# Kernel optimization log

Measured on AMD Instinct MI355X. Metric: run time of the kernel, lower is better.

The kernel has to match this reference:

```python
import jax, jax.numpy as jnp
import numpy as np

PI = 3.141592653589793


def conv2d(x, w, b=None, padding=0, groups=1):
    out = jax.lax.conv_general_dilated(
        x, w, window_strides=(1, 1), padding=((padding, padding), (padding, padding)),
        dimension_numbers=('NCHW', 'OIHW', 'NCHW'), feature_group_count=groups)
    if b is not None:
        out = out + b.reshape(1, -1, 1, 1)
    return out


def group_norm(x, weight, bias, num_groups, eps=1e-5):
    B, C, H, W = x.shape
    xg = x.reshape(B, num_groups, C // num_groups, H, W)
    mean = xg.mean(axis=(2, 3, 4), keepdims=True)
    var = xg.var(axis=(2, 3, 4), keepdims=True)
    xg = (xg - mean) / jnp.sqrt(var + eps)
    return xg.reshape(B, C, H, W) * weight.reshape(1, -1, 1, 1) + bias.reshape(1, -1, 1, 1)


def l2norm(x, eps=1e-12):
    n = jnp.sqrt(jnp.sum(x * x, axis=1, keepdims=True))
    return x / jnp.maximum(n, eps)


def dense_sift(x):
    # kornia DenseSIFTDescriptor defaults: 8 angle bins, 4x4 spatial bins, bin size 4,
    # stride 1, padding 1, rootsift=True, clipval=0.2. Input (B,1,H,W) -> (B,128,H,W).
    eps = 1e-10
    B, C, H, W = x.shape
    # spatial_gradient(x, 'diff'), normalized: central differences / 2, replicate pad
    p = jnp.pad(x, ((0, 0), (0, 0), (1, 1), (1, 1)), mode='edge')
    gx = (p[:, :, 1:-1, 2:] - p[:, :, 1:-1, :-2]) * 0.5
    gy = (p[:, :, 2:, 1:-1] - p[:, :, :-2, 1:-1]) * 0.5
    mag = jnp.sqrt(gx * gx + gy * gy + eps)
    ori = jnp.arctan2(gy, gx + eps) + 2.0 * PI
    o_big = 8.0 * ori / (2.0 * PI)
    bo0f = jnp.floor(o_big)
    wo1 = o_big - bo0f
    bo0 = bo0f % 8
    bo1 = (bo0 + 1) % 8
    wo0m = (1.0 - wo1) * mag
    wo1m = wo1 * mag
    bins = jnp.arange(8, dtype=x.dtype).reshape(1, 8, 1, 1)
    # soft orientation-histogram binning -> (B,8,H,W)
    ang = jnp.where(bo0 == bins, wo0m, 0.0) + jnp.where(bo1 == bins, wo1m, 0.0)
    # triangular bin pooling kernel (ksize=4), depthwise conv, pad 2 -> (B,8,H+1,W+1)
    ks2 = 2.0
    xc2 = ks2 - jnp.abs(jnp.arange(4, dtype=x.dtype) + 0.5 - ks2)
    pk = jnp.outer(xc2, xc2) / (ks2 ** 2)
    pk = jnp.tile(pk.reshape(1, 1, 4, 4), (8, 1, 1, 1))
    pooled = jax.lax.conv_general_dilated(
        ang, pk, (1, 1), ((2, 2), (2, 2)),
        dimension_numbers=('NCHW', 'OIHW', 'NCHW'), feature_group_count=8)
    # PoolingConv with identity reshape kernel (k=4, pad=1) == 4x4 patch extraction
    pp = jnp.pad(pooled, ((0, 0), (0, 0), (1, 1), (1, 1)))
    patches = jnp.stack([pp[:, :, y:y + H, xx:xx + W]
                         for y in range(4) for xx in range(4)], axis=2)  # (B,8,16,H,W)
    out = patches.reshape(B, 128, H, W)
    out = jnp.clip(l2norm(out), 0.0, 0.2)
    out = l2norm(out)
    # rootsift: sqrt(L1-normalized + eps)
    l1 = jnp.sum(jnp.abs(out), axis=1, keepdims=True)
    out = jnp.sqrt(out / jnp.maximum(l1, 1e-12) + eps)
    return out


def gauss1d(ks, sigma):
    t = jnp.arange(ks, dtype=jnp.float32) - (ks - 1) / 2.0
    g = jnp.exp(-(t * t) / (2.0 * sigma * sigma))
    return g / g.sum()


def joint_bilateral_blur(inp, guidance, ks=5, sigma_color=0.1, sigma_space=(1.5, 1.5)):
    # kornia joint_bilateral_blur: border_type='reflect', color_distance_type='l1'
    B, C, H, W = inp.shape
    pad = ks // 2
    pi_ = jnp.pad(inp, ((0, 0), (0, 0), (pad, pad), (pad, pad)), mode='reflect')
    pg = jnp.pad(guidance, ((0, 0), (0, 0), (pad, pad), (pad, pad)), mode='reflect')

    def unfold(p):  # (B,C,H,W,ks*ks), flatten order (dy, dx)
        return jnp.stack([p[:, :, y:y + H, x:x + W]
                          for y in range(ks) for x in range(ks)], axis=-1)

    ui = unfold(pi_)
    ug = unfold(pg)
    diff = ug - guidance[..., None]
    cdist_sq = jnp.square(jnp.sum(jnp.abs(diff), axis=1, keepdims=True))  # L1 over channels, squared
    color_k = jnp.exp(-0.5 / (sigma_color ** 2) * cdist_sq)               # (B,1,H,W,K2)
    space_k = jnp.outer(gauss1d(ks, sigma_space[0]), gauss1d(ks, sigma_space[1])).reshape(1, 1, 1, 1, -1)
    kernel = space_k * color_k
    return (ui * kernel).sum(-1) / kernel.sum(-1)


def setup_inputs() -> dict:
    key = jax.random.key(0)
    ks = jax.random.split(key, 8)
    B, H, W = 4, 270, 512

    def wgt(k, shape, scale=0.05):
        return jax.random.normal(k, shape, dtype=jnp.float32) * scale

    z = lambda n: jnp.zeros((n,), dtype=jnp.float32)
    o = lambda n: jnp.ones((n,), dtype=jnp.float32)
    return {
        'x': jax.random.normal(ks[0], (B, 1, H, W), dtype=jnp.float32),
        'w1': wgt(ks[1], (64, 128, 5, 5)), 'b1': z(64), 'g1w': o(64), 'g1b': z(64),
        'w2': wgt(ks[2], (32, 64, 3, 3)), 'b2': z(32), 'g2w': o(32), 'g2b': z(32),
        'w3': wgt(ks[3], (16, 32, 3, 3)), 'b3': z(16), 'g3w': o(16), 'g3b': z(16),
        'w4': wgt(ks[4], (8, 16, 3, 3)), 'b4': z(8), 'g4w': o(8), 'g4b': z(8),
        'w5': wgt(ks[5], (2, 8, 3, 3)), 'b5': z(2),
        'sw1': wgt(ks[6], (32, 128, 1, 1)), 'sb1': z(32),
        'sw2': wgt(ks[7], (8, 32, 1, 1)), 'sb2': z(8),
    }


def reference(x, w1, b1, g1w, g1b, w2, b2, g2w, g2b, w3, b3, g3w, g3b,
              w4, b4, g4w, g4b, w5, b5, sw1, sb1, sw2, sb2):
    orig = x
    s = dense_sift(x)                                     # (B,128,H,W)
    h = jax.nn.relu(group_norm(conv2d(s, w1, b1, 2), g1w, g1b, 8))
    h = jax.nn.relu(group_norm(conv2d(h, w2, b2, 1), g2w, g2b, 8))
    h = h + conv2d(s, sw1, sb1, 0)                        # skip 1
    blk = h
    h = jax.nn.relu(group_norm(conv2d(h, w3, b3, 1), g3w, g3b, 4))
    h = jax.nn.relu(group_norm(conv2d(h, w4, b4, 1), g4w, g4b, 4))
    h = h + conv2d(blk, sw2, sb2, 0)                      # skip 2
    h = conv2d(h, w5, b5, 1)                              # (B,2,H,W)
    guide = jnp.tile(orig, (1, 2, 1, 1))
    h = joint_bilateral_blur(h, guide, ks=5, sigma_color=0.1, sigma_space=(1.5, 1.5))
    h = jnp.tanh(h)
    scale = jnp.array([0.436, 0.615], dtype=h.dtype).reshape(1, 2, 1, 1)
    return h * scale
```

## Files before the change

### kernel.cpp

```cpp
#include <hip/hip_runtime.h>

#define DEV __device__ __forceinline__

typedef __bf16 bf16x8 __attribute__((ext_vector_type(8)));
typedef float f32x4 __attribute__((ext_vector_type(4)));

union U8 { uint4 q; unsigned short u[8]; };

constexpr int BN = 4, H = 270, W = 512, HW = H * W;
constexpr int IH5 = 274, P5 = 516;
constexpr int IH3 = 272, P3 = 514;

DEV unsigned short f2bf(float f) {
  unsigned int u = __builtin_bit_cast(unsigned int, f);
  u = (u + 0x7FFFu + ((u >> 16) & 1u)) >> 16;
  return (unsigned short)u;
}
DEV float bf2f(unsigned short h) {
  return __builtin_bit_cast(float, (unsigned int)h << 16);
}

#define GLL16(g, l)                                                                        \
  __builtin_amdgcn_global_load_lds((const __attribute__((address_space(1))) void*)(g),     \
                                   (__attribute__((address_space(3))) void*)(l), 16, 0, 0)

DEV int swz(int row) { return ((row >> 1) & 3) << 4; }

__global__ void k_fill(float* __restrict__ out, int n, float v) {
  int i = blockIdx.x * 256 + threadIdx.x;
  if (i < n) out[i] = v;
}

template <int C, int PD>
__global__ void k_halo(unsigned short* __restrict__ buf, int IHt, int pitch, int nb_) {
  int vPerRow = pitch * C / 8;
  int topBot = 2 * PD * vPerRow;
  int sideV = PD * C / 8;
  int midRows = IHt - 2 * PD;
  int perS = topBot + midRows * 2 * sideV;
  int v = blockIdx.x * 256 + threadIdx.x;
  if (v >= nb_ * perS) return;
  int s = v / perS, r = v % perS;
  size_t base = (size_t)s * IHt * pitch * C;
  size_t off;
  if (r < topBot) {
    int half = r / (PD * vPerRow);
    int rr = r % (PD * vPerRow);
    off = ((size_t)(half ? (IHt - PD) : 0) * pitch * C) + (size_t)rr * 8;
  } else {
    int r2 = r - topBot;
    int row = r2 / (2 * sideV), c2 = r2 % (2 * sideV);
    int side = c2 / sideV, cc = c2 % sideV;
    off = ((size_t)(PD + row) * pitch + (side ? (pitch - PD) : 0)) * C + (size_t)cc * 8;
  }
  *(uint4*)(buf + base + off) = uint4{0, 0, 0, 0};
}

__global__ void k_sift_ang(const float* __restrict__ x, float* __restrict__ ang, int nTot) {
  int p = blockIdx.x * 256 + threadIdx.x;
  if (p >= nTot) return;
  int b = p / HW, r = p % HW, y = r / W, xx = r % W;
  const float* xb = x + (size_t)b * HW;
  float xm = xb[y * W + (xx > 0 ? xx - 1 : 0)];
  float xp = xb[y * W + (xx < W - 1 ? xx + 1 : W - 1)];
  float ym = xb[(y > 0 ? y - 1 : 0) * W + xx];
  float yp = xb[(y < H - 1 ? y + 1 : H - 1) * W + xx];
  float gx = (xp - xm) * 0.5f, gy = (yp - ym) * 0.5f;
  float mag = sqrtf(gx * gx + gy * gy + 1e-10f);
  float ori = atan2f(gy, gx + 1e-10f) + 6.2831855f;
  float o = (8.0f * ori) / 6.2831855f;
  float bo0f = floorf(o);
  float wo1 = o - bo0f;
  int b0 = ((int)bo0f) & 7;
  int b1 = (b0 + 1) & 7;
  float w0m = (1.0f - wo1) * mag, w1m = wo1 * mag;
  float v[8];
#pragma unroll
  for (int k = 0; k < 8; ++k)
    v[k] = (k == b0 ? w0m : 0.0f) + (k == b1 ? w1m : 0.0f);
  float4* o4 = (float4*)(ang + (size_t)p * 8);
  o4[0] = make_float4(v[0], v[1], v[2], v[3]);
  o4[1] = make_float4(v[4], v[5], v[6], v[7]);
}

__global__ void k_sift_pool(const float* __restrict__ ang, float* __restrict__ pooled, int nTot) {
  constexpr int PH = H + 1, PW = W + 1;
  int p = blockIdx.x * 256 + threadIdx.x;
  if (p >= nTot) return;
  int b = p / (PH * PW), r = p % (PH * PW), y = r / PW, xx = r % PW;
  float4 a0 = {0, 0, 0, 0}, a1 = {0, 0, 0, 0};
  const float xc2[4] = {0.5f, 1.5f, 1.5f, 0.5f};
#pragma unroll
  for (int ky = 0; ky < 4; ++ky) {
    int yy = y - 2 + ky;
    if (yy < 0 || yy >= H) continue;
#pragma unroll
    for (int kx = 0; kx < 4; ++kx) {
      int xs = xx - 2 + kx;
      if (xs < 0 || xs >= W) continue;
      float w = xc2[ky] * xc2[kx] * 0.25f;
      const float4* s4 = (const float4*)(ang + ((size_t)(b * H + yy) * W + xs) * 8);
      float4 v0 = s4[0], v1 = s4[1];
      a0.x += w * v0.x; a0.y += w * v0.y; a0.z += w * v0.z; a0.w += w * v0.w;
      a1.x += w * v1.x; a1.y += w * v1.y; a1.z += w * v1.z; a1.w += w * v1.w;
    }
  }
  float4* o4 = (float4*)(pooled + (size_t)p * 8);
  o4[0] = a0; o4[1] = a1;
}

__global__ void k_sift_desc(const float* __restrict__ pooled, unsigned short* __restrict__ spad) {
  constexpr int PH = H + 1, PW = W + 1;
  int tid = threadIdx.x;
  int wv = tid >> 6, lane = tid & 63;
  int p = blockIdx.x * 4 + wv;
  int b = p / HW, r = p % HW, yy = r / W, xx = r % W;
  int a = lane >> 3, jj = lane & 7;
  int j0 = jj * 2;
  int dy = j0 >> 2, dx = j0 & 3;
  int rr = yy + dy - 1;
  int c0 = xx + dx - 1, c1 = c0 + 1;
  bool rv = (rr >= 0 && rr <= H);
  int rc = min(max(rr, 0), H);
  const float* pb = pooled + ((size_t)(b * PH + rc) * PW) * 8 + a;
  float v0 = 0.0f, v1 = 0.0f;
  if (rv && c0 >= 0 && c0 <= W) v0 = pb[(size_t)c0 * 8];
  if (rv && c1 >= 0 && c1 <= W) v1 = pb[(size_t)c1 * 8];

  float n2 = v0 * v0 + v1 * v1;
#pragma unroll
  for (int m = 1; m < 64; m <<= 1) n2 += __shfl_xor(n2, m);
  float inv = 1.0f / fmaxf(sqrtf(n2), 1e-12f);
  v0 = fminf(v0 * inv, 0.2f);
  v1 = fminf(v1 * inv, 0.2f);
  float n2b = v0 * v0 + v1 * v1;
#pragma unroll
  for (int m = 1; m < 64; m <<= 1) n2b += __shfl_xor(n2b, m);
  inv = 1.0f / fmaxf(sqrtf(n2b), 1e-12f);
  v0 *= inv; v1 *= inv;
  float l1 = v0 + v1;
#pragma unroll
  for (int m = 1; m < 64; m <<= 1) l1 += __shfl_xor(l1, m);
  float il1 = 1.0f / fmaxf(l1, 1e-12f);
  v0 = sqrtf(v0 * il1 + 1e-10f);
  v1 = sqrtf(v1 * il1 + 1e-10f);
  unsigned int pk = (unsigned int)f2bf(v0) | ((unsigned int)f2bf(v1) << 16);
  *(unsigned int*)(spad + ((size_t)(b * IH5 + yy + 2) * P5 + xx + 2) * 128 + lane * 2) = pk;
}

template <int CIN, int COUT, int KS>
__global__ void k_prep(const float* __restrict__ w, unsigned short* __restrict__ wbuf) {
  int i = blockIdx.x * 256 + threadIdx.x;
  if (i >= KS * KS * COUT * CIN) return;
  int t = i / (COUT * CIN), r2 = i % (COUT * CIN), co = r2 / CIN, e = r2 % CIN;
  wbuf[i] = f2bf(w[(co * CIN + e) * (KS * KS) + t]);
}

template <int CIN, int COUT, int KS, int NG, int PADOFF, int MINB>
__launch_bounds__(256, MINB)
__global__ void k_convr(const unsigned short* __restrict__ in, int IHt, int ipitch,
                        const unsigned short* __restrict__ wtap,
                        const float* __restrict__ bias,
                        unsigned short* __restrict__ outraw,
                        float* __restrict__ part, int nbid) {
  constexpr int SLABPX = 512 + KS - 1;
  constexpr int KQ = CIN / 32;
  constexpr int NF = COUT / 16;
  constexpr int SLAB = SLABPX * 64;
  constexpr int SWQ = COUT * 64;
  constexpr int SWROW = KS * SWQ;
  __shared__ __align__(16) unsigned char slabB[2][SLAB];
  __shared__ __align__(16) unsigned char wrowB[2][SWROW];
  __shared__ float red[4][16];

  int tid = threadIdx.x;
  int lane = tid & 63, wid = tid >> 6;
  int l15 = lane & 15, hi = lane >> 4;

  int bid = blockIdx.x;
  int q8 = nbid >> 3, r8 = nbid & 7;
  int xcd = bid & 7;
  int by = (xcd < r8 ? xcd * (q8 + 1) : r8 * (q8 + 1) + (xcd - r8) * q8) + (bid >> 3);
  int y = by % H, b = by / H;

  f32x4 acc[8][NF] = {};

  auto stage = [&](int it, int pbuf) {
    int q = it / KS, ky = it % KS;
    const char* src = (const char*)(in + ((size_t)(b * IHt + y + ky + PADOFF) * ipitch + PADOFF) * CIN + q * 32);
    for (int d = tid * 16; d < SLAB; d += 4096) {
      int px = d >> 6, qb = d & 63;
      GLL16(src + px * (CIN * 2) + (qb ^ swz(px)), slabB[pbuf] + d);
    }
    const char* wsrc = (const char*)wtap + (size_t)(ky * KS) * (COUT * CIN * 2) + q * 64;
    for (int d = tid * 16; d < SWROW; d += 4096) {
      int kx = d / SWQ, rem = d % SWQ;
      int co = rem >> 6, qb = rem & 63;
      GLL16(wsrc + (size_t)kx * (COUT * CIN * 2) + co * (CIN * 2) + (qb ^ swz(co)), wrowB[pbuf] + d);
    }
  };

  stage(0, 0);
  __syncthreads();

#pragma unroll 1
  for (int it = 0; it < KQ * KS; ++it) {
    int cur = it & 1;
    if (it + 1 < KQ * KS) stage(it + 1, cur ^ 1);
    const unsigned char* sl = slabB[cur];
    const unsigned char* wr = wrowB[cur];
    int koff = hi * 16;
#pragma unroll
    for (int kx = 0; kx < KS; ++kx) {
      bf16x8 af[8];
#pragma unroll
      for (int mi = 0; mi < 8; ++mi) {
        int px = wid * 128 + mi * 16 + l15 + kx;
        af[mi] = *(const bf16x8*)(sl + px * 64 + (koff ^ swz(px)));
      }
#pragma unroll
      for (int ni = 0; ni < NF; ++ni) {
        int co = ni * 16 + l15;
        bf16x8 bq = *(const bf16x8*)(wr + kx * SWQ + co * 64 + (koff ^ swz(co)));
#pragma unroll
        for (int mi = 0; mi < 8; ++mi)
          acc[mi][ni] = __builtin_amdgcn_mfma_f32_16x16x32_bf16(af[mi], bq, acc[mi][ni], 0, 0, 0);
      }
    }
    __syncthreads();
  }

#pragma unroll
  for (int ni = 0; ni < NF; ++ni) {
    float bv = bias[ni * 16 + l15];
#pragma unroll
    for (int mi = 0; mi < 8; ++mi)
#pragma unroll
      for (int rr = 0; rr < 4; ++rr)
        acc[mi][ni][rr] += bv;
  }
  unsigned short* op = outraw + ((size_t)(b * H + y) * W) * COUT;
#pragma unroll
  for (int mi = 0; mi < 8; ++mi)
#pragma unroll
    for (int rr = 0; rr < 4; ++rr) {
      int px = wid * 128 + mi * 16 + hi * 4 + rr;
#pragma unroll
      for (int ni = 0; ni < NF; ++ni)
        op[(size_t)px * COUT + ni * 16 + l15] = f2bf(acc[mi][ni][rr]);
    }
  if constexpr (NG > 0) {
    constexpr int GPC = COUT / NG;
#pragma unroll
    for (int ni = 0; ni < NF; ++ni) {
      float s = 0.0f, q2 = 0.0f;
#pragma unroll
      for (int mi = 0; mi < 8; ++mi)
#pragma unroll
        for (int rr = 0; rr < 4; ++rr) {
          float v = acc[mi][ni][rr];
          s += v; q2 += v * v;
        }
      s += __shfl_xor(s, 16); q2 += __shfl_xor(q2, 16);
      s += __shfl_xor(s, 32); q2 += __shfl_xor(q2, 32);
#pragma unroll
      for (int m = 1; m < GPC; m <<= 1) { s += __shfl_xor(s, m); q2 += __shfl_xor(q2, m); }
      if (hi == 0 && (l15 % GPC) == 0) {
        int g = ni * (16 / GPC) + l15 / GPC;
        red[wid][g] = s;
        red[wid][NG + g] = q2;
      }
    }
    __syncthreads();
    if (tid < 2 * NG)
      part[(size_t)by * (2 * NG) + tid] =
          red[0][tid] + red[1][tid] + red[2][tid] + red[3][tid];
  }
}

template <int COUT, int NG>
__global__ void k_gn_fin(const float* __restrict__ part, int NB,
                         const float* __restrict__ gw, const float* __restrict__ gb,
                         float* __restrict__ scale, float* __restrict__ shift, float invN) {
  constexpr int GPC = COUT / NG;
  int b = blockIdx.x / NG, g = blockIdx.x % NG;
  int lane = threadIdx.x;
  float s = 0.0f, q = 0.0f;
  for (int i = lane; i < NB; i += 64) {
    const float* pp = part + (size_t)(b * NB + i) * (2 * NG);
    s += pp[g]; q += pp[NG + g];
  }
#pragma unroll
  for (int m = 1; m < 64; m <<= 1) { s += __shfl_xor(s, m); q += __shfl_xor(q, m); }
  if (lane == 0) {
    float mean = s * invN;
    float var = q * invN - mean * mean;
    float rstd = rsqrtf(var + 1e-5f);
#pragma unroll
    for (int j = 0; j < GPC; ++j) {
      int c = g * GPC + j;
      float sc = gw[c] * rstd;
      scale[b * COUT + c] = sc;
      shift[b * COUT + c] = gb[c] - mean * sc;
    }
  }
}

template <int C, bool ADDSKIP>
__global__ void k_norm(const unsigned short* __restrict__ raw,
                       const unsigned short* __restrict__ skip,
                       const float* __restrict__ scale, const float* __restrict__ shift,
                       unsigned short* __restrict__ outpad) {
  int e = blockIdx.x * 256 + threadIdx.x;
  int idx = e * 8;
  int p = idx / C, c0 = idx % C;
  int b = p / HW, r = p % HW, y = r / W, xx = r % W;
  U8 v; v.q = *(const uint4*)(raw + (size_t)p * C + c0);
  U8 sk;
  if (ADDSKIP) sk.q = *(const uint4*)(skip + (size_t)p * C + c0);
  const float* sc = scale + b * C + c0;
  const float* sh = shift + b * C + c0;
  U8 o;
#pragma unroll
  for (int j = 0; j < 8; ++j) {
    float f = fmaxf(bf2f(v.u[j]) * sc[j] + sh[j], 0.0f);
    if (ADDSKIP) f += bf2f(sk.u[j]);
    o.u[j] = f2bf(f);
  }
  *(uint4*)(outpad + ((size_t)(b * IH3 + y + 1) * P3 + xx + 1) * C + c0) = o.q;
}

__global__ void k_conv4(const unsigned short* __restrict__ h3pad, const float* __restrict__ w4,
                        const float* __restrict__ b4, unsigned short* __restrict__ h4raw,
                        float* __restrict__ part) {
  __shared__ float wl[1152];
  __shared__ float red[4][8];
  for (int i = threadIdx.x; i < 1152; i += 256) {
    int t = i / 128, r2 = i % 128, ci = r2 >> 3, co = r2 & 7;
    wl[i] = w4[(co * 16 + ci) * 9 + t];
  }
  __syncthreads();
  int p = blockIdx.x * 256 + threadIdx.x;
  int b = p / HW, r = p % HW, y = r / W, xx = r % W;
  float acc[8];
#pragma unroll
  for (int co = 0; co < 8; ++co) acc[co] = b4[co];
#pragma unroll
  for (int t = 0; t < 9; ++t) {
    int ky = t / 3, kx = t % 3;
    const unsigned short* ip = h3pad + ((size_t)(b * IH3 + y + ky) * P3 + (xx + kx)) * 16;
    U8 u0, u1;
    u0.q = *(const uint4*)ip;
    u1.q = *(const uint4*)(ip + 8);
#pragma unroll
    for (int ci = 0; ci < 16; ++ci) {
      float iv = bf2f(ci < 8 ? u0.u[ci] : u1.u[ci - 8]);
#pragma unroll
      for (int co = 0; co < 8; ++co)
        acc[co] += iv * wl[t * 128 + ci * 8 + co];
    }
  }
  int lane = threadIdx.x & 63, wv = threadIdx.x >> 6;
  float s[4], q[4];
#pragma unroll
  for (int g = 0; g < 4; ++g) {
    s[g] = acc[2 * g] + acc[2 * g + 1];
    q[g] = acc[2 * g] * acc[2 * g] + acc[2 * g + 1] * acc[2 * g + 1];
  }
#pragma unroll
  for (int m = 1; m < 64; m <<= 1) {
#pragma unroll
    for (int g = 0; g < 4; ++g) { s[g] += __shfl_xor(s[g], m); q[g] += __shfl_xor(q[g], m); }
  }
  if (lane == 0) {
#pragma unroll
    for (int g = 0; g < 4; ++g) { red[wv][g] = s[g]; red[wv][4 + g] = q[g]; }
  }
  __syncthreads();
  if (threadIdx.x < 8)
    part[(size_t)blockIdx.x * 8 + threadIdx.x] =
        red[0][threadIdx.x] + red[1][threadIdx.x] + red[2][threadIdx.x] + red[3][threadIdx.x];
  U8 o;
#pragma unroll
  for (int co = 0; co < 8; ++co) o.u[co] = f2bf(acc[co]);
  *(uint4*)(h4raw + (size_t)p * 8) = o.q;
}

__global__ void k_norm4(const unsigned short* __restrict__ h4raw, const unsigned short* __restrict__ blkpad,
                        const float* __restrict__ scale, const float* __restrict__ shift,
                        const float* __restrict__ sw2, const float* __restrict__ sb2,
                        unsigned short* __restrict__ blk2pad) {
  __shared__ float wl[256];
  {
    int i = threadIdx.x;
    int ci = i >> 3, co = i & 7;
    wl[i] = sw2[co * 32 + ci];
  }
  __syncthreads();
  int p = blockIdx.x * 256 + threadIdx.x;
  int b = p / HW, r = p % HW, y = r / W, xx = r % W;
  float acc[8];
#pragma unroll
  for (int co = 0; co < 8; ++co) acc[co] = sb2[co];
  size_t cbase = ((size_t)(b * IH3 + y + 1) * P3 + (xx + 1));
  const unsigned short* bp = blkpad + cbase * 32;
#pragma unroll
  for (int half = 0; half < 4; ++half) {
    U8 u; u.q = *(const uint4*)(bp + half * 8);
#pragma unroll
    for (int j = 0; j < 8; ++j) {
      float iv = bf2f(u.u[j]);
      int ci = half * 8 + j;
#pragma unroll
      for (int co = 0; co < 8; ++co) acc[co] += iv * wl[ci * 8 + co];
    }
  }
  U8 hv; hv.q = *(const uint4*)(h4raw + (size_t)p * 8);
  U8 o;
#pragma unroll
  for (int co = 0; co < 8; ++co) {
    float f = fmaxf(bf2f(hv.u[co]) * scale[b * 8 + co] + shift[b * 8 + co], 0.0f) + acc[co];
    o.u[co] = f2bf(f);
  }
  *(uint4*)(blk2pad + cbase * 8) = o.q;
}

__global__ void k_conv5(const unsigned short* __restrict__ blk2pad, const float* __restrict__ w5,
                        const float* __restrict__ b5, float* __restrict__ h5) {
  __shared__ float wl[144];
  if (threadIdx.x < 144) {
    int i = threadIdx.x;
    int t = i / 16, r2 = i % 16, ci = r2 >> 1, co = r2 & 1;
    wl[i] = w5[(co * 8 + ci) * 9 + t];
  }
  __syncthreads();
  int p = blockIdx.x * 256 + threadIdx.x;
  int b = p / HW, r = p % HW, y = r / W, xx = r % W;
  float a0 = b5[0], a1 = b5[1];
#pragma unroll
  for (int t = 0; t < 9; ++t) {
    int ky = t / 3, kx = t % 3;
    const unsigned short* ip = blk2pad + ((size_t)(b * IH3 + y + ky) * P3 + (xx + kx)) * 8;
    U8 u; u.q = *(const uint4*)ip;
#pragma unroll
    for (int ci = 0; ci < 8; ++ci) {
      float iv = bf2f(u.u[ci]);
      a0 += iv * wl[t * 16 + ci * 2];
      a1 += iv * wl[t * 16 + ci * 2 + 1];
    }
  }
  h5[(size_t)p * 2] = a0;
  h5[(size_t)p * 2 + 1] = a1;
}

__global__ void k_bilateral(const float* __restrict__ h5, const float* __restrict__ x,
                            float* __restrict__ out, int nTot) {
  int p = blockIdx.x * 256 + threadIdx.x;
  if (p >= nTot) return;
  int b = p / HW, r = p % HW, y = r / W, xx = r % W;
  const float* xb = x + (size_t)b * HW;
  float xc = xb[r];
  float e1 = expf(-1.0f / 4.5f), e0 = expf(-4.0f / 4.5f);
  float gs = 1.0f + 2.0f * e1 + 2.0f * e0;
  float g[5] = {e0 / gs, e1 / gs, 1.0f / gs, e1 / gs, e0 / gs};
  float n0 = 0.0f, n1 = 0.0f, den = 0.0f;
#pragma unroll
  for (int dy = 0; dy < 5; ++dy) {
    int yn = y + dy - 2;
    yn = yn < 0 ? -yn : (yn >= H ? 2 * H - 2 - yn : yn);
#pragma unroll
    for (int dx = 0; dx < 5; ++dx) {
      int xn = xx + dx - 2;
      xn = xn < 0 ? -xn : (xn >= W ? 2 * W - 2 - xn : xn);
      float xv = xb[yn * W + xn];
      float d = xv - xc;
      float wgt = g[dy] * g[dx] * expf(-200.0f * d * d);
      den += wgt;
      const float* hp = h5 + ((size_t)(b * HW) + yn * W + xn) * 2;
      n0 += wgt * hp[0];
      n1 += wgt * hp[1];
    }
  }
  float o0 = tanhf(n0 / den) * 0.436f;
  float o1 = tanhf(n1 / den) * 0.615f;
  out[(size_t)(b * 2) * HW + r] = o0;
  out[(size_t)(b * 2 + 1) * HW + r] = o1;
}

extern "C" void kernel_launch(void* const* d_in, const int* in_sizes, int n_in,
                              void* d_out, int out_size, void* d_ws, size_t ws_size,
                              hipStream_t stream) {
  (void)in_sizes; (void)n_in; (void)out_size;
  const float* x   = (const float*)d_in[0];
  const float* w1  = (const float*)d_in[1];
  const float* b1  = (const float*)d_in[2];
  const float* g1w = (const float*)d_in[3];
  const float* g1b = (const float*)d_in[4];
  const float* w2  = (const float*)d_in[5];
  const float* b2  = (const float*)d_in[6];
  const float* g2w = (const float*)d_in[7];
  const float* g2b = (const float*)d_in[8];
  const float* w3  = (const float*)d_in[9];
  const float* b3  = (const float*)d_in[10];
  const float* g3w = (const float*)d_in[11];
  const float* g3b = (const float*)d_in[12];
  const float* w4  = (const float*)d_in[13];
  const float* b4  = (const float*)d_in[14];
  const float* g4w = (const float*)d_in[15];
  const float* g4b = (const float*)d_in[16];
  const float* w5  = (const float*)d_in[17];
  const float* b5  = (const float*)d_in[18];
  const float* sw1 = (const float*)d_in[19];
  const float* sb1 = (const float*)d_in[20];
  const float* sw2 = (const float*)d_in[21];
  const float* sb2 = (const float*)d_in[22];
  float* out = (float*)d_out;
  char* ws = (char*)d_ws;

  auto AL = [](size_t v) { return (v + 255) & ~(size_t)255; };
  const size_t sSPAD  = (size_t)IH5 * P5 * 128 * 2;
  const size_t sANG   = (size_t)HW * 8 * 4;
  const size_t sH1RAW = (size_t)HW * 64 * 2;
  const size_t sH1PAD = (size_t)IH3 * P3 * 64 * 2;
  const size_t sH2RAW = (size_t)HW * 32 * 2;
  const size_t sBLKP  = (size_t)IH3 * P3 * 32 * 2;
  const size_t sH3RAW = (size_t)HW * 16 * 2;
  const size_t sH3PAD = (size_t)IH3 * P3 * 16 * 2;
  const size_t sH4RAW = (size_t)HW * 8 * 2;
  const size_t sBLK2  = (size_t)IH3 * P3 * 8 * 2;

  int nb = 0;
  size_t offB = 0, offH1PAD = 0, offSmall = 0;
  const size_t smallFixed = AL(1024 * 1024) + AL((size_t)4 * 1080 * 16 * 4) + 8 * 4096;
  for (int cand = 4; cand >= 1; cand >>= 1) {
    size_t oB   = AL((size_t)cand * sSPAD);
    size_t oH1P = AL(oB + (size_t)cand * sH1RAW);
    size_t oS   = AL(oH1P + (size_t)cand * sH1PAD);
    size_t need = oS + smallFixed + AL((size_t)cand * sH2RAW);
    if (ws_size >= need) { nb = cand; offB = oB; offH1PAD = oH1P; offSmall = oS; break; }
  }
  if (nb == 0) {
    k_fill<<<(BN * 2 * HW + 255) / 256, 256, 0, stream>>>(out, BN * 2 * HW, 123.0f);
    return;
  }

  size_t oWB1  = offSmall;
  size_t oWB2  = AL(oWB1 + 25 * 64 * 128 * 2);
  size_t oWB3  = AL(oWB2 + 9 * 32 * 64 * 2);
  size_t oWBS  = AL(oWB3 + 9 * 16 * 32 * 2);
  size_t oPART = AL(oWBS + 32 * 128 * 2);
  size_t oSC1  = AL(oPART + (size_t)4 * 1080 * 16 * 4);
  size_t oSC2  = oSC1 + 4096, oSC3 = oSC2 + 4096, oSC4 = oSC3 + 4096;
  size_t oSK1  = oSC4 + 4096;

  unsigned short* wb1  = (unsigned short*)(ws + oWB1);
  unsigned short* wb2  = (unsigned short*)(ws + oWB2);
  unsigned short* wb3  = (unsigned short*)(ws + oWB3);
  unsigned short* wbs1 = (unsigned short*)(ws + oWBS);
  float* part = (float*)(ws + oPART);
  float* sc1 = (float*)(ws + oSC1); float* sh1 = sc1 + nb * 64;
  float* sc2 = (float*)(ws + oSC2); float* sh2 = sc2 + nb * 32;
  float* sc3 = (float*)(ws + oSC3); float* sh3 = sc3 + nb * 16;
  float* sc4 = (float*)(ws + oSC4); float* sh4 = sc4 + nb * 8;
  unsigned short* sk1 = (unsigned short*)(ws + oSK1);

  k_prep<128, 64, 5><<<800, 256, 0, stream>>>(w1, wb1);
  k_prep<64, 32, 3><<<72, 256, 0, stream>>>(w2, wb2);
  k_prep<32, 16, 3><<<18, 256, 0, stream>>>(w3, wb3);
  k_prep<128, 32, 1><<<16, 256, 0, stream>>>(sw1, wbs1);

  size_t t0 = AL((size_t)nb * sBLKP);
  size_t t1 = AL(t0 + (size_t)nb * sH3RAW);
  size_t t2 = AL(t1 + (size_t)nb * sH3PAD);
  size_t t3 = AL(t2 + (size_t)nb * sH4RAW);
  size_t t4 = AL(t3 + (size_t)nb * sBLK2);

  for (int b0 = 0; b0 < BN; b0 += nb) {
    const float* x_c = x + (size_t)b0 * HW;
    float* out_c = out + (size_t)b0 * 2 * HW;
    unsigned short* spad   = (unsigned short*)(ws);
    float*          ang    = (float*)(ws + offB);
    float*          pooled = (float*)(ws + AL(offB + (size_t)nb * sANG));
    unsigned short* h1raw  = (unsigned short*)(ws + offB);
    unsigned short* h1pad  = (unsigned short*)(ws + offH1PAD);
    unsigned short* h2raw  = (unsigned short*)(ws + offB);
    unsigned short* blkpad = (unsigned short*)(ws);
    unsigned short* h3raw  = (unsigned short*)(ws + t0);
    unsigned short* h3pad  = (unsigned short*)(ws + t1);
    unsigned short* h4raw  = (unsigned short*)(ws + t2);
    unsigned short* blk2   = (unsigned short*)(ws + t3);
    float*          h5     = (float*)(ws + t4);
    int nHW = nb * HW;
    int nbid = nb * H;

    k_halo<128, 2><<<(nb * 50304 + 255) / 256, 256, 0, stream>>>(spad, IH5, P5, nb);
    k_halo<64, 1><<<(nb * 12544 + 255) / 256, 256, 0, stream>>>(h1pad, IH3, P3, nb);

    k_sift_ang<<<nb * 540, 256, 0, stream>>>(x_c, ang, nHW);
    int nPP = nb * (H + 1) * (W + 1);
    k_sift_pool<<<(nPP + 255) / 256, 256, 0, stream>>>(ang, pooled, nPP);
    k_sift_desc<<<nHW / 4, 256, 0, stream>>>(pooled, spad);

    k_convr<128, 64, 5, 8, 0, 1><<<nbid, 256, 0, stream>>>(spad, IH5, P5, wb1, b1, h1raw, part, nbid);
    k_gn_fin<64, 8><<<nb * 8, 64, 0, stream>>>(part, H, g1w, g1b, sc1, sh1, 1.0f / (8.0f * HW));
    k_norm<64, false><<<nb * 4320, 256, 0, stream>>>(h1raw, nullptr, sc1, sh1, h1pad);

    k_convr<64, 32, 3, 8, 0, 2><<<nbid, 256, 0, stream>>>(h1pad, IH3, P3, wb2, b2, h2raw, part, nbid);
    k_gn_fin<32, 8><<<nb * 8, 64, 0, stream>>>(part, H, g2w, g2b, sc2, sh2, 1.0f / (4.0f * HW));
    k_convr<128, 32, 1, 0, 2, 2><<<nbid, 256, 0, stream>>>(spad, IH5, P5, wbs1, sb1, sk1, nullptr, nbid);

    k_halo<32, 1><<<(nb * 6272 + 255) / 256, 256, 0, stream>>>(blkpad, IH3, P3, nb);
    k_halo<16, 1><<<(nb * 3136 + 255) / 256, 256, 0, stream>>>(h3pad, IH3, P3, nb);
    k_halo<8, 1><<<(nb * 1568 + 255) / 256, 256, 0, stream>>>(blk2, IH3, P3, nb);

    k_norm<32, true><<<nb * 2160, 256, 0, stream>>>(h2raw, sk1, sc2, sh2, blkpad);

    k_convr<32, 16, 3, 4, 0, 2><<<nbid, 256, 0, stream>>>(blkpad, IH3, P3, wb3, b3, h3raw, part, nbid);
    k_gn_fin<16, 4><<<nb * 4, 64, 0, stream>>>(part, H, g3w, g3b, sc3, sh3, 1.0f / (4.0f * HW));
    k_norm<16, false><<<nb * 1080, 256, 0, stream>>>(h3raw, nullptr, sc3, sh3, h3pad);

    k_conv4<<<nb * 540, 256, 0, stream>>>(h3pad, w4, b4, h4raw, part);
    k_gn_fin<8, 4><<<nb * 4, 64, 0, stream>>>(part, 540, g4w, g4b, sc4, sh4, 1.0f / (2.0f * HW));
    k_norm4<<<nb * 540, 256, 0, stream>>>(h4raw, blkpad, sc4, sh4, sw2, sb2, blk2);

    k_conv5<<<nb * 540, 256, 0, stream>>>(blk2, w5, b5, h5);
    k_bilateral<<<nb * 540, 256, 0, stream>>>(h5, x_c, out_c, nHW);
  }
}
```

Baseline: 807.2 us.

## Fuse 1x1 skip conv into 5x5 conv1 and use 512-thread conv blocks

Folds the 1x1 skip convolution on the SIFT descriptor into the first 5x5 conv kernel. At the centre tap it issues extra MFMAs on the slab fragments already in LDS, so the separate launch and its re-read of the 128-channel padded descriptor go away. All conv kernels now run with 512 threads (8 waves of 64 pixels each, not 4 waves of 128), which halves per-wave accumulators and raises occupancy hints. The cost is fewer MFMAs per LDS fragment load, a small extra LDS buffer for the skip weights, and more waves contending for LDS.

```diff
diff --git a/kernel.cpp b/kernel.cpp
--- a/kernel.cpp
+++ b/kernel.cpp
@@ -156,12 +156,15 @@
   wbuf[i] = f2bf(w[(co * CIN + e) * (KS * KS) + t]);
 }
 
-template <int CIN, int COUT, int KS, int NG, int PADOFF, int MINB>
-__launch_bounds__(256, MINB)
+template <int CIN, int COUT, int KS, int NG, int PADOFF, int MINB, bool FSKIP>
+__launch_bounds__(512, MINB)
 __global__ void k_convr(const unsigned short* __restrict__ in, int IHt, int ipitch,
                         const unsigned short* __restrict__ wtap,
                         const float* __restrict__ bias,
+                        const unsigned short* __restrict__ wsk,
+                        const float* __restrict__ skb,
                         unsigned short* __restrict__ outraw,
+                        unsigned short* __restrict__ skraw,
                         float* __restrict__ part, int nbid) {
   constexpr int SLABPX = 512 + KS - 1;
   constexpr int KQ = CIN / 32;
@@ -169,9 +172,11 @@
   constexpr int SLAB = SLABPX * 64;
   constexpr int SWQ = COUT * 64;
   constexpr int SWROW = KS * SWQ;
+  constexpr int SSK = FSKIP ? 32 * 64 : 16;
   __shared__ __align__(16) unsigned char slabB[2][SLAB];
   __shared__ __align__(16) unsigned char wrowB[2][SWROW];
-  __shared__ float red[4][16];
+  __shared__ __align__(16) unsigned char wskB[2][SSK];
+  __shared__ float red[8][16];
 
   int tid = threadIdx.x;
   int lane = tid & 63, wid = tid >> 6;
@@ -183,39 +188,52 @@
   int by = (xcd < r8 ? xcd * (q8 + 1) : r8 * (q8 + 1) + (xcd - r8) * q8) + (bid >> 3);
   int y = by % H, b = by / H;
 
-  f32x4 acc[8][NF] = {};
+  f32x4 acc[4][NF] = {};
+  f32x4 ask[4][2] = {};
 
   auto stage = [&](int it, int pbuf) {
     int q = it / KS, ky = it % KS;
     const char* src = (const char*)(in + ((size_t)(b * IHt + y + ky + PADOFF) * ipitch + PADOFF) * CIN + q * 32);
-    for (int d = tid * 16; d < SLAB; d += 4096) {
+    for (int d = tid * 16; d < SLAB; d += 8192) {
       int px = d >> 6, qb = d & 63;
       GLL16(src + px * (CIN * 2) + (qb ^ swz(px)), slabB[pbuf] + d);
     }
     const char* wsrc = (const char*)wtap + (size_t)(ky * KS) * (COUT * CIN * 2) + q * 64;
-    for (int d = tid * 16; d < SWROW; d += 4096) {
+    for (int d = tid * 16; d < SWROW; d += 8192) {
       int kx = d / SWQ, rem = d % SWQ;
       int co = rem >> 6, qb = rem & 63;
       GLL16(wsrc + (size_t)kx * (COUT * CIN * 2) + co * (CIN * 2) + (qb ^ swz(co)), wrowB[pbuf] + d);
     }
   };
+  auto stage_wsk = [&](int q, int pbuf) {
+    const char* src = (const char*)wsk + q * 64;
+    for (int d = tid * 16; d < 32 * 64; d += 8192) {
+      int co = d >> 6, qb = d & 63;
+      GLL16(src + co * (CIN * 2) + (qb ^ swz(co)), wskB[pbuf] + d);
+    }
+  };
 
   stage(0, 0);
+  if constexpr (FSKIP) stage_wsk(0, 0);
   __syncthreads();
 
 #pragma unroll 1
   for (int it = 0; it < KQ * KS; ++it) {
     int cur = it & 1;
-    if (it + 1 < KQ * KS) stage(it + 1, cur ^ 1);
+    int q = it / KS, ky = it % KS;
+    if (it + 1 < KQ * KS) {
+      stage(it + 1, cur ^ 1);
+      if (FSKIP && (it + 1) % KS == 0) stage_wsk((it + 1) / KS, ((it + 1) / KS) & 1);
+    }
     const unsigned char* sl = slabB[cur];
     const unsigned char* wr = wrowB[cur];
     int koff = hi * 16;
 #pragma unroll
     for (int kx = 0; kx < KS; ++kx) {
-      bf16x8 af[8];
-#pragma unroll
-      for (int mi = 0; mi < 8; ++mi) {
-        int px = wid * 128 + mi * 16 + l15 + kx;
+      bf16x8 af[4];
+#pragma unroll
+      for (int mi = 0; mi < 4; ++mi) {
+        int px = wid * 64 + mi * 16 + l15 + kx;
         af[mi] = *(const bf16x8*)(sl + px * 64 + (koff ^ swz(px)));
       }
 #pragma unroll
@@ -223,9 +241,21 @@
         int co = ni * 16 + l15;
         bf16x8 bq = *(const bf16x8*)(wr + kx * SWQ + co * 64 + (koff ^ swz(co)));
 #pragma unroll
-        for (int mi = 0; mi < 8; ++mi)
+        for (int mi = 0; mi < 4; ++mi)
           acc[mi][ni] = __builtin_amdgcn_mfma_f32_16x16x32_bf16(af[mi], bq, acc[mi][ni], 0, 0, 0);
       }
+      if constexpr (FSKIP) {
+        if (ky == KS / 2 && kx == KS / 2) {
+#pragma unroll
+          for (int ni = 0; ni < 2; ++ni) {
+            int co = ni * 16 + l15;
+            bf16x8 bq = *(const bf16x8*)(wskB[q & 1] + co * 64 + (koff ^ swz(co)));
+#pragma unroll
+            for (int mi = 0; mi < 4; ++mi)
+              ask[mi][ni] = __builtin_amdgcn_mfma_f32_16x16x32_bf16(af[mi], bq, ask[mi][ni], 0, 0, 0);
+          }
+        }
+      }
     }
     __syncthreads();
   }
@@ -234,28 +264,49 @@
   for (int ni = 0; ni < NF; ++ni) {
     float bv = bias[ni * 16 + l15];
 #pragma unroll
-    for (int mi = 0; mi < 8; ++mi)
+    for (int mi = 0; mi < 4; ++mi)
 #pragma unroll
       for (int rr = 0; rr < 4; ++rr)
         acc[mi][ni][rr] += bv;
   }
   unsigned short* op = outraw + ((size_t)(b * H + y) * W) * COUT;
 #pragma unroll
-  for (int mi = 0; mi < 8; ++mi)
+  for (int mi = 0; mi < 4; ++mi)
 #pragma unroll
     for (int rr = 0; rr < 4; ++rr) {
-      int px = wid * 128 + mi * 16 + hi * 4 + rr;
+      int px = wid * 64 + mi * 16 + hi * 4 + rr;
 #pragma unroll
       for (int ni = 0; ni < NF; ++ni)
         op[(size_t)px * COUT + ni * 16 + l15] = f2bf(acc[mi][ni][rr]);
     }
+  if constexpr (FSKIP) {
+    unsigned short* ops = skraw + ((size_t)(b * H + y) * W) * 32;
+#pragma unroll
+    for (int ni = 0; ni < 2; ++ni) {
+      float bv = skb[ni * 16 + l15];
+#pragma unroll
+      for (int mi = 0; mi < 4; ++mi)
+#pragma unroll
+        for (int rr = 0; rr < 4; ++rr)
+          ask[mi][ni][rr] += bv;
+    }
+#pragma unroll
+    for (int mi = 0; mi < 4; ++mi)
+#pragma unroll
+      for (int rr = 0; rr < 4; ++rr) {
+        int px = wid * 64 + mi * 16 + hi * 4 + rr;
+#pragma unroll
+        for (int ni = 0; ni < 2; ++ni)
+          ops[(size_t)px * 32 + ni * 16 + l15] = f2bf(ask[mi][ni][rr]);
+      }
+  }
   if constexpr (NG > 0) {
     constexpr int GPC = COUT / NG;
 #pragma unroll
     for (int ni = 0; ni < NF; ++ni) {
       float s = 0.0f, q2 = 0.0f;
 #pragma unroll
-      for (int mi = 0; mi < 8; ++mi)
+      for (int mi = 0; mi < 4; ++mi)
 #pragma unroll
         for (int rr = 0; rr < 4; ++rr) {
           float v = acc[mi][ni][rr];
@@ -272,9 +323,12 @@
       }
     }
     __syncthreads();
-    if (tid < 2 * NG)
-      part[(size_t)by * (2 * NG) + tid] =
-          red[0][tid] + red[1][tid] + red[2][tid] + red[3][tid];
+    if (tid < 2 * NG) {
+      float t = 0.0f;
+#pragma unroll
+      for (int wv2 = 0; wv2 < 8; ++wv2) t += red[wv2][tid];
+      part[(size_t)by * (2 * NG) + tid] = t;
+    }
   }
 }
 
@@ -601,13 +655,14 @@
     k_sift_pool<<<(nPP + 255) / 256, 256, 0, stream>>>(ang, pooled, nPP);
     k_sift_desc<<<nHW / 4, 256, 0, stream>>>(pooled, spad);
 
-    k_convr<128, 64, 5, 8, 0, 1><<<nbid, 256, 0, stream>>>(spad, IH5, P5, wb1, b1, h1raw, part, nbid);
+    k_convr<128, 64, 5, 8, 0, 2, true><<<nbid, 512, 0, stream>>>(
+        spad, IH5, P5, wb1, b1, wbs1, sb1, h1raw, sk1, part, nbid);
     k_gn_fin<64, 8><<<nb * 8, 64, 0, stream>>>(part, H, g1w, g1b, sc1, sh1, 1.0f / (8.0f * HW));
     k_norm<64, false><<<nb * 4320, 256, 0, stream>>>(h1raw, nullptr, sc1, sh1, h1pad);
 
-    k_convr<64, 32, 3, 8, 0, 2><<<nbid, 256, 0, stream>>>(h1pad, IH3, P3, wb2, b2, h2raw, part, nbid);
+    k_convr<64, 32, 3, 8, 0, 4, false><<<nbid, 512, 0, stream>>>(
+        h1pad, IH3, P3, wb2, b2, nullptr, nullptr, h2raw, nullptr, part, nbid);
     k_gn_fin<32, 8><<<nb * 8, 64, 0, stream>>>(part, H, g2w, g2b, sc2, sh2, 1.0f / (4.0f * HW));
-    k_convr<128, 32, 1, 0, 2, 2><<<nbid, 256, 0, stream>>>(spad, IH5, P5, wbs1, sb1, sk1, nullptr, nbid);
 
     k_halo<32, 1><<<(nb * 6272 + 255) / 256, 256, 0, stream>>>(blkpad, IH3, P3, nb);
     k_halo<16, 1><<<(nb * 3136 + 255) / 256, 256, 0, stream>>>(h3pad, IH3, P3, nb);
@@ -615,7 +670,8 @@
 
     k_norm<32, true><<<nb * 2160, 256, 0, stream>>>(h2raw, sk1, sc2, sh2, blkpad);
 
-    k_convr<32, 16, 3, 4, 0, 2><<<nbid, 256, 0, stream>>>(blkpad, IH3, P3, wb3, b3, h3raw, part, nbid);
+    k_convr<32, 16, 3, 4, 0, 4, false><<<nbid, 512, 0, stream>>>(
+        blkpad, IH3, P3, wb3, b3, nullptr, nullptr, h3raw, nullptr, part, nbid);
     k_gn_fin<16, 4><<<nb * 4, 64, 0, stream>>>(part, H, g3w, g3b, sc3, sh3, 1.0f / (4.0f * HW));
     k_norm<16, false><<<nb * 1080, 256, 0, stream>>>(h3raw, nullptr, sc3, sh3, h3pad);
 
```

Result: faster. 729.0 us (-9.7%).
